# Kernel optimization log

Hardware: AMD Instinct MI355X
Metric: run time of the kernel (lower is better)

Reference implementation:

```python
import jax, jax.numpy as jnp
import numpy as np

SEQ_LEN = 16384
D = 2048
K = 50          # tagset size
START = 48
STOP = 49
NEG = -10000.0


def setup_inputs() -> dict:
    key = jax.random.key(0)
    k1, k2, k3, k4 = jax.random.split(key, 4)
    input_var = jax.random.normal(k1, (SEQ_LEN, D), jnp.float32)
    tags = jax.random.randint(k2, (SEQ_LEN,), 0, 48, dtype=jnp.int32)  # real tags only
    W = jax.random.normal(k3, (K, D), jnp.float32) * 0.02              # hidden2tag weight
    b = jnp.zeros((K,), jnp.float32)                                   # hidden2tag bias
    transitions = jax.random.normal(k4, (K, K), jnp.float32) * 0.1
    # match the torch init: no transition into START, none out of STOP
    transitions = transitions.at[START, :].set(NEG).at[:, STOP].set(NEG)
    return {"input_var": input_var, "tags": tags, "W": W, "b": b, "transitions": transitions}


def reference(input_var, tags, W, b, transitions):
    # dropout in eval mode == identity (faithful deterministic forward)
    feats = input_var @ W.T + b  # [T, K] emission scores

    # --- CRF forward algorithm (log partition) ---
    alpha0 = jnp.full((K,), NEG, jnp.float32).at[START].set(0.0)

    def step(alpha, feat):
        # tag_var[i, j] = alpha[j] + transitions[i, j] + feat[i]
        s = alpha[None, :] + transitions           # [K, K]
        m = jnp.max(s, axis=1)                     # stable log-sum-exp
        alpha_new = feat + m + jnp.log(jnp.sum(jnp.exp(s - m[:, None]), axis=1))
        return alpha_new, None

    alpha, _ = jax.lax.scan(step, alpha0, feats)
    term = alpha + transitions[STOP]
    mt = jnp.max(term)
    forward_score = mt + jnp.log(jnp.sum(jnp.exp(term - mt)))

    # --- gold path score ---
    pad_start = jnp.concatenate([jnp.array([START], dtype=tags.dtype), tags])
    pad_stop = jnp.concatenate([tags, jnp.array([STOP], dtype=tags.dtype)])
    gold = (jnp.sum(transitions[pad_stop, pad_start])
            + jnp.sum(feats[jnp.arange(SEQ_LEN), tags]))

    return forward_score - gold
```

## Files before the change

kernel.cpp:

```cpp
#include <hip/hip_runtime.h>

typedef unsigned short u16;
typedef unsigned int u32;
typedef __bf16 b16x8 __attribute__((ext_vector_type(8)));
typedef float f32x16 __attribute__((ext_vector_type(16)));

#define SEQ   16384
#define DM    2048
#define KT    50
#define NST   48
#define NSP   49

__device__ __forceinline__ int perm64(int g){
  int q = (g>>2)&3;
  return (q==1 || q==2) ? (g^12) : g;
}
__device__ __forceinline__ u16 bfb(float f){
  __bf16 b = (__bf16)f;
  return __builtin_bit_cast(u16, b);
}
__device__ __forceinline__ int pk2(float a, float b){
  return (int)((u32)bfb(a) | ((u32)bfb(b) << 16));
}
__device__ __forceinline__ b16x8 cast8(int4 v){ return __builtin_bit_cast(b16x8, v); }

__device__ __forceinline__ f32x16 mfma_(b16x8 a, b16x8 b, f32x16 c){
  return __builtin_amdgcn_mfma_f32_32x32x16_bf16(a, b, c, 0, 0, 0);
}

__device__ __forceinline__ void mm64(const b16x8 A[2][4], const b16x8 B[4][2], f32x16 acc[2][2]){
#pragma unroll
  for (int mi=0; mi<2; ++mi)
#pragma unroll
    for (int ni=0; ni<2; ++ni){
      f32x16 a;
#pragma unroll
      for (int q=0;q<16;q++) a[q] = 0.0f;
#pragma unroll
      for (int kt=0; kt<4; ++kt) a = mfma_(A[mi][kt], B[kt][ni], a);
      acc[mi][ni] = a;
    }
}

__device__ __forceinline__ void repack(const f32x16 acc[2][2], b16x8 B[4][2]){
#pragma unroll
  for (int kb=0; kb<4; ++kb){
    const int mi = kb>>1, t = kb&1;
#pragma unroll
    for (int ni=0; ni<2; ++ni){
      int4 dw;
      dw.x = pk2(acc[mi][ni][8*t+0], acc[mi][ni][8*t+1]);
      dw.y = pk2(acc[mi][ni][8*t+2], acc[mi][ni][8*t+3]);
      dw.z = pk2(acc[mi][ni][8*t+4], acc[mi][ni][8*t+5]);
      dw.w = pk2(acc[mi][ni][8*t+6], acc[mi][ni][8*t+7]);
      B[kb][ni] = cast8(dw);
    }
  }
}
__device__ __forceinline__ void repack_s(const f32x16 acc[2][2], b16x8 B[4][2], float s){
#pragma unroll
  for (int kb=0; kb<4; ++kb){
    const int mi = kb>>1, t = kb&1;
#pragma unroll
    for (int ni=0; ni<2; ++ni){
      int4 dw;
      dw.x = pk2(acc[mi][ni][8*t+0]*s, acc[mi][ni][8*t+1]*s);
      dw.y = pk2(acc[mi][ni][8*t+2]*s, acc[mi][ni][8*t+3]*s);
      dw.z = pk2(acc[mi][ni][8*t+4]*s, acc[mi][ni][8*t+5]*s);
      dw.w = pk2(acc[mi][ni][8*t+6]*s, acc[mi][ni][8*t+7]*s);
      B[kb][ni] = cast8(dw);
    }
  }
}

template<int PERM>
__device__ __forceinline__ void ident_frags(b16x8 B[4][2], int lane){
  const int h = lane>>5, j0 = lane&31;
#pragma unroll
  for (int kt=0; kt<4; ++kt)
#pragma unroll
    for (int ni=0; ni<2; ++ni){
      const int col = j0 + 32*ni;
      int d[4];
#pragma unroll
      for (int dd=0; dd<4; ++dd){
        int r0 = 16*kt + 8*h + 2*dd, r1 = r0 + 1;
        int p0 = PERM ? perm64(r0) : r0;
        int p1 = PERM ? perm64(r1) : r1;
        d[dd] = (int)((p0==col ? 0x3F80u : 0u) | ((p1==col ? 0x3F80u : 0u) << 16));
      }
      int4 v; v.x=d[0]; v.y=d[1]; v.z=d[2]; v.w=d[3];
      B[kt][ni] = cast8(v);
    }
}

__device__ __forceinline__ float acc_wave_max(const f32x16 acc[2][2]){
  float m = 0.0f;
#pragma unroll
  for (int mi=0;mi<2;mi++)
#pragma unroll
    for (int ni=0;ni<2;ni++)
#pragma unroll
      for (int q=0;q<16;q++) m = fmaxf(m, acc[mi][ni][q]);
#pragma unroll
  for (int o=32;o>=1;o>>=1) m = fmaxf(m, __shfl_xor(m, o, 64));
  return m;
}

template<int PROW, int PCOL>
__device__ __forceinline__ void store_mat_lds(u16* mat, const f32x16 acc[2][2], float inv, int lane){
  const int h = lane>>5, j0 = lane&31;
#pragma unroll
  for (int mi=0;mi<2;mi++)
#pragma unroll
    for (int ni=0;ni<2;ni++)
#pragma unroll
      for (int r=0;r<16;r++){
        int gp = 32*mi + (r&3) + 8*(r>>2) + 4*h;
        int a = PROW ? perm64(gp) : gp;
        int cc = 32*ni + j0;
        int b = PCOL ? perm64(cc) : cc;
        mat[a*64 + (b ^ ((a&7)<<3))] = bfb(acc[mi][ni][r]*inv);
      }
}
template<int PROW, int PCOL>
__device__ __forceinline__ void store_mat_glob(u16* mat, const f32x16 acc[2][2], float inv, int lane){
  const int h = lane>>5, j0 = lane&31;
#pragma unroll
  for (int mi=0;mi<2;mi++)
#pragma unroll
    for (int ni=0;ni<2;ni++)
#pragma unroll
      for (int r=0;r<16;r++){
        int gp = 32*mi + (r&3) + 8*(r>>2) + 4*h;
        int a = PROW ? perm64(gp) : gp;
        int cc = 32*ni + j0;
        int b = PCOL ? perm64(cc) : cc;
        mat[a*64 + b] = bfb(acc[mi][ni][r]*inv);
      }
}
__device__ __forceinline__ void load_afrag_lds(const u16* mat, b16x8 A[2][4], int lane){
  const int h = lane>>5, i0 = lane&31;
#pragma unroll
  for (int mi=0;mi<2;mi++)
#pragma unroll
    for (int kt=0;kt<4;kt++){
      int i = 32*mi + i0;
      int cb = (16*kt + 8*h) ^ ((i&7)<<3);
      A[mi][kt] = cast8(*(const int4*)(mat + i*64 + cb));
    }
}
__device__ __forceinline__ void load_afrag_glob(const u16* mat, b16x8 A[2][4], int lane){
  const int h = lane>>5, i0 = lane&31;
#pragma unroll
  for (int mi=0;mi<2;mi++)
#pragma unroll
    for (int kt=0;kt<4;kt++){
      int i = 32*mi + i0;
      A[mi][kt] = cast8(*(const int4*)(mat + i*64 + 16*kt + 8*h));
    }
}

__global__ __launch_bounds__(512, 2) void k_fused(const float* __restrict__ in,
      const int* __restrict__ tags, const float* __restrict__ W,
      const float* __restrict__ bias, const float* __restrict__ T,
      float* __restrict__ gpart, u16* __restrict__ M1, float* __restrict__ S1){
  __shared__ __align__(16) char smem[66560];
  u16* const bA = (u16*)smem;
  u16* const bB = (u16*)(smem + 32768);
  __shared__ float logs_l[8];
  const int t = threadIdx.x;
  const int w = t>>6, lane = t&63;
  const int j0 = lane&31, h = lane>>5;
  const int rh = w&1, ch = (w>>1)&1, kq = (w>>2)&1;
  const int row0 = blockIdx.x*64;
  const int aswz = (j0&7)<<3;

  float rA[2][8], rB[2][8];
  f32x16 acc;
#pragma unroll
  for (int q=0;q<16;q++) acc[q]=0.f;

#define LOADCHUNK(kc)                                                       \
  { _Pragma("unroll")                                                       \
    for (int i=0;i<2;i++){                                                  \
      int g=(i<<9)+t; int r=g>>4, c8=g&15;                                  \
      const float* p = in + (size_t)(row0+r)*DM + (kc)*128 + c8*8;          \
      float4 f0=*(const float4*)p, f1=*(const float4*)(p+4);                \
      rA[i][0]=f0.x; rA[i][1]=f0.y; rA[i][2]=f0.z; rA[i][3]=f0.w;           \
      rA[i][4]=f1.x; rA[i][5]=f1.y; rA[i][6]=f1.z; rA[i][7]=f1.w;           \
      if (r < KT){                                                          \
        const float* q2 = W + (size_t)r*DM + (kc)*128 + c8*8;               \
        float4 g0=*(const float4*)q2, g1=*(const float4*)(q2+4);            \
        rB[i][0]=g0.x; rB[i][1]=g0.y; rB[i][2]=g0.z; rB[i][3]=g0.w;         \
        rB[i][4]=g1.x; rB[i][5]=g1.y; rB[i][6]=g1.z; rB[i][7]=g1.w;         \
      } else {                                                              \
        _Pragma("unroll") for (int z=0;z<8;z++) rB[i][z]=0.f;               \
      }                                                                     \
    } }
#define WRITECHUNK(d)                                                       \
  { _Pragma("unroll")                                                       \
    for (int i=0;i<2;i++){                                                  \
      int g=(i<<9)+t; int r=g>>4, c8=g&15;                                  \
      int off = r*128 + ((c8*8) ^ ((r&7)<<3));                              \
      int4 da; da.x=pk2(rA[i][0],rA[i][1]); da.y=pk2(rA[i][2],rA[i][3]);    \
      da.z=pk2(rA[i][4],rA[i][5]); da.w=pk2(rA[i][6],rA[i][7]);             \
      *(int4*)(bA + (d)*8192 + off) = da;                                   \
      int4 db; db.x=pk2(rB[i][0],rB[i][1]); db.y=pk2(rB[i][2],rB[i][3]);    \
      db.z=pk2(rB[i][4],rB[i][5]); db.w=pk2(rB[i][6],rB[i][7]);             \
      *(int4*)(bB + (d)*8192 + off) = db;                                   \
    } }

  LOADCHUNK(0); WRITECHUNK(0);
  __syncthreads();
  for (int kc=0; kc<16; ++kc){
    const int d = kc & 1;
    if (kc < 15) LOADCHUNK(kc+1);
    const u16* Arow = bA + d*8192 + (32*rh + j0)*128;
    const u16* Brow = bB + d*8192 + (32*ch + j0)*128;
#pragma unroll
    for (int kk=0;kk<4;kk++){
      const int kt = kq*4 + kk;
      b16x8 aF = cast8(*(const int4*)(Arow + ((kt*16 + h*8) ^ aswz)));
      b16x8 bF = cast8(*(const int4*)(Brow + ((kt*16 + h*8) ^ aswz)));
      acc = mfma_(aF, bF, acc);
    }
    if (kc < 15) WRITECHUNK(d^1);
    __syncthreads();
  }
#undef LOADCHUNK
#undef WRITECHUNK

  float* planes = (float*)smem;
  float* tile   = (float*)(smem + 32768);
  float* mrow   = (float*)(smem + 49664);
  float* ue     = (float*)(smem + 50176);
  u16*   tmats  = (u16*)  smem;
#pragma unroll
  for (int r=0;r<16;r++){
    int gp = (r&3) + 8*(r>>2) + 4*h;
    planes[kq*4096 + (32*rh + gp)*64 + 32*ch + j0] = acc[r];
  }
  float E32[2][4][8];
  {
    const int pr = perm64(j0);
#pragma unroll
    for (int mi=0;mi<2;mi++){
      const int prow = 32*mi + pr;
#pragma unroll
      for (int kt=0;kt<4;kt++)
#pragma unroll
        for (int j=0;j<8;j++){
          const int c = 16*kt + 8*h + j;
          E32[mi][kt][j] = (prow < KT && c < KT) ? __expf(T[prow*50 + c]) : 0.f;
        }
    }
  }
  __syncthreads();
  for (int cidx = t; cidx < 4096; cidx += 512){
    int g = cidx>>6, c = cidx&63;
    float v = planes[cidx] + planes[4096 + cidx];
    tile[g*66 + c] = (c<KT) ? (v + bias[c]) : -1e4f;
  }
  __syncthreads();
  if (t < 64){
    int g = t;
    float mx = -1e30f;
    for (int c=0;c<KT;c++) mx = fmaxf(mx, tile[g*66+c]);
    mrow[g] = mx;
    int tt = row0 + g;
    int s1 = tags[tt];
    int s0 = (tt==0) ? NST : tags[tt-1];
    float part = (tile[g*66 + s1] - mx) + T[s1*50 + s0];
    if (tt == SEQ-1) part += T[NSP*50 + s1];
#pragma unroll
    for (int o=32;o>=1;o>>=1) part += __shfl_xor(part, o, 64);
    if (t==0) gpart[blockIdx.x] = part;
  }
  __syncthreads();
  for (int cidx = t; cidx < 4096; cidx += 512){
    int g = cidx>>6, c = cidx&63;
    ue[cidx] = __expf(tile[g*66 + c] - mrow[g]);
  }
  __syncthreads();

  b16x8 Bf[4][2];
  ident_frags<0>(Bf, lane);
  f32x16 sacc[2][2];
  {
    const int pr = perm64(j0);
    const int tr0 = w*8;
#pragma unroll 1
    for (int s=0;s<8;s++){
      float u0 = ue[(tr0+s)*64 + pr];
      float u1 = ue[(tr0+s)*64 + 32 + pr];
      b16x8 Af[2][4];
#pragma unroll
      for (int mi=0;mi<2;mi++){
        const float uu = mi ? u1 : u0;
#pragma unroll
        for (int kt=0;kt<4;kt++){
          int4 dw;
          dw.x = pk2(uu*E32[mi][kt][0], uu*E32[mi][kt][1]);
          dw.y = pk2(uu*E32[mi][kt][2], uu*E32[mi][kt][3]);
          dw.z = pk2(uu*E32[mi][kt][4], uu*E32[mi][kt][5]);
          dw.w = pk2(uu*E32[mi][kt][6], uu*E32[mi][kt][7]);
          Af[mi][kt] = cast8(dw);
        }
      }
      mm64(Af, Bf, sacc);
      repack(sacc, Bf);
    }
  }
  float m = acc_wave_max(sacc);
  float sl = __logf(m);
  float inv = 1.0f/m;
  int active = 1;
#pragma unroll 1
  for (int l=0; l<3; ++l){
    const int storer = active && ((w>>l)&1);
    if (active && lane==0) logs_l[w] = sl;
    if (storer){
      store_mat_lds<0,0>(tmats + (w>>(l+1))*4096, sacc, inv, lane);
    } else if (active){
      repack_s(sacc, Bf, inv);
    }
    __syncthreads();
    if (active && !storer){
      b16x8 Am[2][4];
      load_afrag_lds(tmats + (w>>(l+1))*4096, Am, lane);
      mm64(Am, Bf, sacc);
      sl += logs_l[w + (1<<l)];
      m = acc_wave_max(sacc);
      sl += __logf(m);
      inv = 1.0f/m;
    }
    if (storer) active = 0;
    __syncthreads();
  }
  if (w==0){
    store_mat_glob<1,0>(M1 + (size_t)blockIdx.x*4096, sacc, inv, lane);
    if (lane==0) S1[blockIdx.x] = sl;
  }
}

__global__ __launch_bounds__(512, 2) void k_final(const u16* __restrict__ M1,
      const float* __restrict__ S1, const float* __restrict__ T,
      const float* __restrict__ gpart, float* __restrict__ out){
  const int t = threadIdx.x;
  const int w = t>>6, lane = t&63;
  const int h = lane>>5;
  __shared__ __align__(16) u16 mats[8][4096];
  __shared__ float logs[8];
  __shared__ float alpha[64];

  {
    const int base = w*32;
    b16x8 Bc[4][2]; ident_frags<1>(Bc, lane);
    f32x16 a2[2][2];
    float sl = 0.f;
    b16x8 A0[2][4], A1[2][4], A2[2][4], A3[2][4];
    load_afrag_glob(M1 + (size_t)(base+0)*4096, A0, lane);
    load_afrag_glob(M1 + (size_t)(base+1)*4096, A1, lane);
    load_afrag_glob(M1 + (size_t)(base+2)*4096, A2, lane);
#pragma unroll 1
    for (int mm=0; mm<32; mm++){
      if (mm<29) load_afrag_glob(M1 + (size_t)(base+mm+3)*4096, A3, lane);
      sl += S1[base+mm];
      mm64(A0, Bc, a2);
      if (mm!=31 && (mm&7)==7){
        float mx = acc_wave_max(a2);
        sl += __logf(mx);
        repack_s(a2, Bc, 1.0f/mx);
      } else {
        repack(a2, Bc);
      }
#pragma unroll
      for (int mi=0;mi<2;mi++)
#pragma unroll
        for (int kt=0;kt<4;kt++){
          A0[mi][kt]=A1[mi][kt]; A1[mi][kt]=A2[mi][kt]; A2[mi][kt]=A3[mi][kt];
        }
    }
    float mx = acc_wave_max(a2);
    sl += __logf(mx);
    store_mat_lds<0,1>(mats[w], a2, 1.0f/mx, lane);
    if (lane==0) logs[w] = sl;
  }
  __syncthreads();
  if (w==0){
    b16x8 Bc[4][2]; ident_frags<1>(Bc, lane);
    f32x16 a2[2][2];
#pragma unroll 1
    for (int m8=0;m8<8;m8++){
      b16x8 Am[2][4];
      load_afrag_lds(mats[m8], Am, lane);
      mm64(Am, Bc, a2);
      repack(a2, Bc);
    }
    float slog = logs[0]+logs[1]+logs[2]+logs[3]+logs[4]+logs[5]+logs[6]+logs[7];
    if ((lane&31)==16){
#pragma unroll
      for (int mi=0;mi<2;mi++)
#pragma unroll
        for (int r=0;r<16;r++){
          int gp = 32*mi + (r&3) + 8*(r>>2) + 4*h;
          alpha[gp] = a2[mi][1][r];
        }
    }
    float gold = gpart[lane] + gpart[lane+64] + gpart[lane+128] + gpart[lane+192];
#pragma unroll
    for (int o=32;o>=1;o>>=1) gold += __shfl_xor(gold, o, 64);
    float a = alpha[lane];
    float term = (lane < KT && a > 0.f) ? (__logf(a) + slog + T[NSP*50 + lane]) : -1e30f;
    float tm = term;
#pragma unroll
    for (int o=32;o>=1;o>>=1) tm = fmaxf(tm, __shfl_xor(tm, o, 64));
    float e = __expf(term - tm);
#pragma unroll
    for (int o=32;o>=1;o>>=1) e += __shfl_xor(e, o, 64);
    if (lane==0) out[0] = (tm + __logf(e)) - gold;
  }
}

extern "C" void kernel_launch(void* const* d_in, const int* in_sizes, int n_in,
                              void* d_out, int out_size, void* d_ws, size_t ws_size,
                              hipStream_t stream) {
  (void)in_sizes; (void)n_in; (void)out_size; (void)ws_size;
  const float* input = (const float*)d_in[0];
  const int*   tags  = (const int*)  d_in[1];
  const float* W     = (const float*)d_in[2];
  const float* bias  = (const float*)d_in[3];
  const float* T     = (const float*)d_in[4];

  char* ws = (char*)d_ws;
  float* gpart = (float*)(ws + 0);
  u16*   M1    = (u16*)  (ws + 1024);
  float* S1    = (float*)(ws + 2098176);

  k_fused<<<256, 512, 0, stream>>>(input, tags, W, bias, T, gpart, M1, S1);
  k_final<<<1,   512, 0, stream>>>(M1, S1, T, gpart, (float*)d_out);
}
```

Baseline: 120.4 us.

## Halve rows per block and split final matrix-product reduction into two-level tree

The fused kernel now processes 32 sequence rows per block instead of 64, across 512 blocks with a four-way K split, smaller shared memory and a higher occupancy hint. The single-block final reduction over 256 transfer matrices is replaced by an 8-block middle kernel and a one-wave last kernel. This targets the serial tail in the one-block reducer and underused CUs in the GEMM phase. The cost is an extra launch, more M1 traffic, and the W tile being re-read by twice as many blocks.

```diff
diff --git a/kernel.cpp b/kernel.cpp
--- a/kernel.cpp
+++ b/kernel.cpp
@@ -161,36 +161,37 @@
     }
 }
 
-__global__ __launch_bounds__(512, 2) void k_fused(const float* __restrict__ in,
+__global__ __launch_bounds__(512, 4) void k_fused(const float* __restrict__ in,
       const int* __restrict__ tags, const float* __restrict__ W,
       const float* __restrict__ bias, const float* __restrict__ T,
       float* __restrict__ gpart, u16* __restrict__ M1, float* __restrict__ S1){
-  __shared__ __align__(16) char smem[66560];
+  __shared__ __align__(16) char smem[49664];
   u16* const bA = (u16*)smem;
-  u16* const bB = (u16*)(smem + 32768);
+  u16* const bB = (u16*)(smem + 16384);
   __shared__ float logs_l[8];
   const int t = threadIdx.x;
   const int w = t>>6, lane = t&63;
   const int j0 = lane&31, h = lane>>5;
-  const int rh = w&1, ch = (w>>1)&1, kq = (w>>2)&1;
-  const int row0 = blockIdx.x*64;
+  const int kq = w>>1, ch = w&1;
+  const int row0 = blockIdx.x*32;
   const int aswz = (j0&7)<<3;
 
-  float rA[2][8], rB[2][8];
+  float rA[8], rB[2][8];
   f32x16 acc;
 #pragma unroll
   for (int q=0;q<16;q++) acc[q]=0.f;
 
 #define LOADCHUNK(kc)                                                       \
-  { _Pragma("unroll")                                                       \
+  { int r=t>>4, c8=t&15;                                                    \
+    const float* p = in + (size_t)(row0+r)*DM + (kc)*128 + c8*8;            \
+    float4 f0=*(const float4*)p, f1=*(const float4*)(p+4);                  \
+    rA[0]=f0.x; rA[1]=f0.y; rA[2]=f0.z; rA[3]=f0.w;                         \
+    rA[4]=f1.x; rA[5]=f1.y; rA[6]=f1.z; rA[7]=f1.w;                         \
+    _Pragma("unroll")                                                       \
     for (int i=0;i<2;i++){                                                  \
-      int g=(i<<9)+t; int r=g>>4, c8=g&15;                                  \
-      const float* p = in + (size_t)(row0+r)*DM + (kc)*128 + c8*8;          \
-      float4 f0=*(const float4*)p, f1=*(const float4*)(p+4);                \
-      rA[i][0]=f0.x; rA[i][1]=f0.y; rA[i][2]=f0.z; rA[i][3]=f0.w;           \
-      rA[i][4]=f1.x; rA[i][5]=f1.y; rA[i][6]=f1.z; rA[i][7]=f1.w;           \
-      if (r < KT){                                                          \
-        const float* q2 = W + (size_t)r*DM + (kc)*128 + c8*8;               \
+      int g=(i<<9)+t; int rr=g>>4, cc8=g&15;                                \
+      if (rr < KT){                                                         \
+        const float* q2 = W + (size_t)rr*DM + (kc)*128 + cc8*8;             \
         float4 g0=*(const float4*)q2, g1=*(const float4*)(q2+4);            \
         rB[i][0]=g0.x; rB[i][1]=g0.y; rB[i][2]=g0.z; rB[i][3]=g0.w;         \
         rB[i][4]=g1.x; rB[i][5]=g1.y; rB[i][6]=g1.z; rB[i][7]=g1.w;         \
@@ -199,13 +200,15 @@
       }                                                                     \
     } }
 #define WRITECHUNK(d)                                                       \
-  { _Pragma("unroll")                                                       \
+  { int r=t>>4, c8=t&15;                                                    \
+    int offA = r*128 + ((c8*8) ^ ((r&7)<<3));                               \
+    int4 da; da.x=pk2(rA[0],rA[1]); da.y=pk2(rA[2],rA[3]);                  \
+    da.z=pk2(rA[4],rA[5]); da.w=pk2(rA[6],rA[7]);                           \
+    *(int4*)(bA + (d)*4096 + offA) = da;                                    \
+    _Pragma("unroll")                                                       \
     for (int i=0;i<2;i++){                                                  \
-      int g=(i<<9)+t; int r=g>>4, c8=g&15;                                  \
-      int off = r*128 + ((c8*8) ^ ((r&7)<<3));                              \
-      int4 da; da.x=pk2(rA[i][0],rA[i][1]); da.y=pk2(rA[i][2],rA[i][3]);    \
-      da.z=pk2(rA[i][4],rA[i][5]); da.w=pk2(rA[i][6],rA[i][7]);             \
-      *(int4*)(bA + (d)*8192 + off) = da;                                   \
+      int g=(i<<9)+t; int rr=g>>4, cc8=g&15;                                \
+      int off = rr*128 + ((cc8*8) ^ ((rr&7)<<3));                           \
       int4 db; db.x=pk2(rB[i][0],rB[i][1]); db.y=pk2(rB[i][2],rB[i][3]);    \
       db.z=pk2(rB[i][4],rB[i][5]); db.w=pk2(rB[i][6],rB[i][7]);             \
       *(int4*)(bB + (d)*8192 + off) = db;                                   \
@@ -216,11 +219,11 @@
   for (int kc=0; kc<16; ++kc){
     const int d = kc & 1;
     if (kc < 15) LOADCHUNK(kc+1);
-    const u16* Arow = bA + d*8192 + (32*rh + j0)*128;
+    const u16* Arow = bA + d*4096 + j0*128;
     const u16* Brow = bB + d*8192 + (32*ch + j0)*128;
 #pragma unroll
-    for (int kk=0;kk<4;kk++){
-      const int kt = kq*4 + kk;
+    for (int kk=0;kk<2;kk++){
+      const int kt = kq*2 + kk;
       b16x8 aF = cast8(*(const int4*)(Arow + ((kt*16 + h*8) ^ aswz)));
       b16x8 bF = cast8(*(const int4*)(Brow + ((kt*16 + h*8) ^ aswz)));
       acc = mfma_(aF, bF, acc);
@@ -233,13 +236,13 @@
 
   float* planes = (float*)smem;
   float* tile   = (float*)(smem + 32768);
-  float* mrow   = (float*)(smem + 49664);
-  float* ue     = (float*)(smem + 50176);
+  float* mrow   = (float*)(smem + 41216);
+  float* ue     = (float*)(smem + 41344);
   u16*   tmats  = (u16*)  smem;
 #pragma unroll
   for (int r=0;r<16;r++){
     int gp = (r&3) + 8*(r>>2) + 4*h;
-    planes[kq*4096 + (32*rh + gp)*64 + 32*ch + j0] = acc[r];
+    planes[kq*2048 + gp*64 + 32*ch + j0] = acc[r];
   }
   float E32[2][4][8];
   {
@@ -257,13 +260,13 @@
     }
   }
   __syncthreads();
-  for (int cidx = t; cidx < 4096; cidx += 512){
+  for (int cidx = t; cidx < 2048; cidx += 512){
     int g = cidx>>6, c = cidx&63;
-    float v = planes[cidx] + planes[4096 + cidx];
+    float v = planes[cidx] + planes[2048+cidx] + planes[4096+cidx] + planes[6144+cidx];
     tile[g*66 + c] = (c<KT) ? (v + bias[c]) : -1e4f;
   }
   __syncthreads();
-  if (t < 64){
+  if (t < 32){
     int g = t;
     float mx = -1e30f;
     for (int c=0;c<KT;c++) mx = fmaxf(mx, tile[g*66+c]);
@@ -274,11 +277,11 @@
     float part = (tile[g*66 + s1] - mx) + T[s1*50 + s0];
     if (tt == SEQ-1) part += T[NSP*50 + s1];
 #pragma unroll
-    for (int o=32;o>=1;o>>=1) part += __shfl_xor(part, o, 64);
+    for (int o=16;o>=1;o>>=1) part += __shfl_xor(part, o, 64);
     if (t==0) gpart[blockIdx.x] = part;
   }
   __syncthreads();
-  for (int cidx = t; cidx < 4096; cidx += 512){
+  for (int cidx = t; cidx < 2048; cidx += 512){
     int g = cidx>>6, c = cidx&63;
     ue[cidx] = __expf(tile[g*66 + c] - mrow[g]);
   }
@@ -289,9 +292,9 @@
   f32x16 sacc[2][2];
   {
     const int pr = perm64(j0);
-    const int tr0 = w*8;
+    const int tr0 = w*4;
 #pragma unroll 1
-    for (int s=0;s<8;s++){
+    for (int s=0;s<4;s++){
       float u0 = ue[(tr0+s)*64 + pr];
       float u1 = ue[(tr0+s)*64 + 32 + pr];
       b16x8 Af[2][4];
@@ -344,43 +347,31 @@
   }
 }
 
-__global__ __launch_bounds__(512, 2) void k_final(const u16* __restrict__ M1,
-      const float* __restrict__ S1, const float* __restrict__ T,
-      const float* __restrict__ gpart, float* __restrict__ out){
+__global__ __launch_bounds__(512) void k_mid(const u16* __restrict__ M1,
+      const float* __restrict__ S1, u16* __restrict__ M2, float* __restrict__ S2){
   const int t = threadIdx.x;
   const int w = t>>6, lane = t&63;
-  const int h = lane>>5;
+  const int j = blockIdx.x;
   __shared__ __align__(16) u16 mats[8][4096];
   __shared__ float logs[8];
-  __shared__ float alpha[64];
-
   {
-    const int base = w*32;
+    const int base = j*64 + w*8;
     b16x8 Bc[4][2]; ident_frags<1>(Bc, lane);
     f32x16 a2[2][2];
     float sl = 0.f;
-    b16x8 A0[2][4], A1[2][4], A2[2][4], A3[2][4];
+    b16x8 A0[2][4], A1[2][4], A2[2][4];
     load_afrag_glob(M1 + (size_t)(base+0)*4096, A0, lane);
     load_afrag_glob(M1 + (size_t)(base+1)*4096, A1, lane);
-    load_afrag_glob(M1 + (size_t)(base+2)*4096, A2, lane);
 #pragma unroll 1
-    for (int mm=0; mm<32; mm++){
-      if (mm<29) load_afrag_glob(M1 + (size_t)(base+mm+3)*4096, A3, lane);
+    for (int mm=0; mm<8; mm++){
+      if (mm<6) load_afrag_glob(M1 + (size_t)(base+mm+2)*4096, A2, lane);
       sl += S1[base+mm];
       mm64(A0, Bc, a2);
-      if (mm!=31 && (mm&7)==7){
-        float mx = acc_wave_max(a2);
-        sl += __logf(mx);
-        repack_s(a2, Bc, 1.0f/mx);
-      } else {
-        repack(a2, Bc);
-      }
+      repack(a2, Bc);
 #pragma unroll
       for (int mi=0;mi<2;mi++)
 #pragma unroll
-        for (int kt=0;kt<4;kt++){
-          A0[mi][kt]=A1[mi][kt]; A1[mi][kt]=A2[mi][kt]; A2[mi][kt]=A3[mi][kt];
-        }
+        for (int kt=0;kt<4;kt++){ A0[mi][kt]=A1[mi][kt]; A1[mi][kt]=A2[mi][kt]; }
     }
     float mx = acc_wave_max(a2);
     sl += __logf(mx);
@@ -399,28 +390,60 @@
       repack(a2, Bc);
     }
     float slog = logs[0]+logs[1]+logs[2]+logs[3]+logs[4]+logs[5]+logs[6]+logs[7];
-    if ((lane&31)==16){
-#pragma unroll
-      for (int mi=0;mi<2;mi++)
-#pragma unroll
-        for (int r=0;r<16;r++){
-          int gp = 32*mi + (r&3) + 8*(r>>2) + 4*h;
-          alpha[gp] = a2[mi][1][r];
-        }
-    }
-    float gold = gpart[lane] + gpart[lane+64] + gpart[lane+128] + gpart[lane+192];
-#pragma unroll
-    for (int o=32;o>=1;o>>=1) gold += __shfl_xor(gold, o, 64);
-    float a = alpha[lane];
-    float term = (lane < KT && a > 0.f) ? (__logf(a) + slog + T[NSP*50 + lane]) : -1e30f;
-    float tm = term;
-#pragma unroll
-    for (int o=32;o>=1;o>>=1) tm = fmaxf(tm, __shfl_xor(tm, o, 64));
-    float e = __expf(term - tm);
-#pragma unroll
-    for (int o=32;o>=1;o>>=1) e += __shfl_xor(e, o, 64);
-    if (lane==0) out[0] = (tm + __logf(e)) - gold;
-  }
+    float m2 = acc_wave_max(a2);
+    slog += __logf(m2);
+    store_mat_glob<0,1>(M2 + (size_t)j*4096, a2, 1.0f/m2, lane);
+    if (lane==0) S2[j] = slog;
+  }
+}
+
+__global__ __launch_bounds__(64) void k_last(const u16* __restrict__ M2,
+      const float* __restrict__ S2, const float* __restrict__ T,
+      const float* __restrict__ gpart, float* __restrict__ out){
+  const int lane = threadIdx.x & 63;
+  const int h = lane>>5;
+  __shared__ float alpha[64];
+  float gold = 0.f;
+#pragma unroll
+  for (int i=0;i<8;i++) gold += gpart[lane + 64*i];
+#pragma unroll
+  for (int o=32;o>=1;o>>=1) gold += __shfl_xor(gold, o, 64);
+
+  b16x8 Bc[4][2]; ident_frags<1>(Bc, lane);
+  f32x16 a2[2][2];
+  float slog = 0.f;
+  b16x8 A0[2][4], A1[2][4], A2[2][4];
+  load_afrag_glob(M2 + (size_t)0*4096, A0, lane);
+  load_afrag_glob(M2 + (size_t)1*4096, A1, lane);
+#pragma unroll 1
+  for (int m8=0;m8<8;m8++){
+    if (m8<6) load_afrag_glob(M2 + (size_t)(m8+2)*4096, A2, lane);
+    slog += S2[m8];
+    mm64(A0, Bc, a2);
+    repack(a2, Bc);
+#pragma unroll
+    for (int mi=0;mi<2;mi++)
+#pragma unroll
+      for (int kt=0;kt<4;kt++){ A0[mi][kt]=A1[mi][kt]; A1[mi][kt]=A2[mi][kt]; }
+  }
+  if ((lane&31)==16){
+#pragma unroll
+    for (int mi=0;mi<2;mi++)
+#pragma unroll
+      for (int r=0;r<16;r++){
+        int gp = 32*mi + (r&3) + 8*(r>>2) + 4*h;
+        alpha[gp] = a2[mi][1][r];
+      }
+  }
+  float a = alpha[lane];
+  float term = (lane < KT && a > 0.f) ? (__logf(a) + slog + T[NSP*50 + lane]) : -1e30f;
+  float tm = term;
+#pragma unroll
+  for (int o=32;o>=1;o>>=1) tm = fmaxf(tm, __shfl_xor(tm, o, 64));
+  float e = __expf(term - tm);
+#pragma unroll
+  for (int o=32;o>=1;o>>=1) e += __shfl_xor(e, o, 64);
+  if (lane==0) out[0] = (tm + __logf(e)) - gold;
 }
 
 extern "C" void kernel_launch(void* const* d_in, const int* in_sizes, int n_in,
@@ -435,9 +458,12 @@
 
   char* ws = (char*)d_ws;
   float* gpart = (float*)(ws + 0);
-  u16*   M1    = (u16*)  (ws + 1024);
-  float* S1    = (float*)(ws + 2098176);
-
-  k_fused<<<256, 512, 0, stream>>>(input, tags, W, bias, T, gpart, M1, S1);
-  k_final<<<1,   512, 0, stream>>>(M1, S1, T, gpart, (float*)d_out);
-}
+  u16*   M1    = (u16*)  (ws + 2048);
+  float* S1    = (float*)(ws + 4196352);
+  u16*   M2    = (u16*)  (ws + 4198400);
+  float* S2    = (float*)(ws + 4263936);
+
+  k_fused<<<512, 512, 0, stream>>>(input, tags, W, bias, T, gpart, M1, S1);
+  k_mid  <<<8,   512, 0, stream>>>(M1, S1, M2, S2);
+  k_last <<<1,   64,  0, stream>>>(M2, S2, T, gpart, (float*)d_out);
+}
```

Measured after the change: 138.2 us. 1.15x slower.
